# Kernel optimization log

Hardware: AMD Instinct MI355X
Metric: run time of the kernel (lower is better)

## Reference

```python
import jax, jax.numpy as jnp
import numpy as np

B, S, D = 16, 4096, 128
FACTOR = 1


def setup_inputs() -> dict:
    key = jax.random.key(0)
    kq, kk, kv = jax.random.split(key, 3)
    Q = jax.random.normal(kq, (B, S, D), dtype=jnp.float32)
    K = jax.random.normal(kk, (B, S, D), dtype=jnp.float32)
    V = jax.random.normal(kv, (B, S, D), dtype=jnp.float32)
    return {"Q": Q, "K": K, "V": V}


def reference(Q, K, V):
    # [B, S, D] -> [B, D, S] (head dim of 1 is elided; all ops are per-(b,d) lane)
    Qc = jnp.transpose(Q, (0, 2, 1))
    Kc = jnp.transpose(K, (0, 2, 1))
    Vc = jnp.transpose(V, (0, 2, 1))
    seq_len = Qc.shape[-1]
    # FFT cross-correlation: corr[b,d,tau] = sum_t Q[b,d,t] K[b,d,t-tau] (circular)
    corr = jnp.fft.irfft(
        jnp.fft.rfft(Qc, axis=-1) * jnp.conj(jnp.fft.rfft(Kc, axis=-1)),
        n=seq_len, axis=-1)  # [B, D, S]
    top_k = int(FACTOR * np.log(seq_len))  # = 8 for S=4096
    weights, delay = jax.lax.top_k(corr, top_k)  # [B, D, K], raw corr values (no softmax)
    # time-delay aggregation: roll V circularly by each selected delay and weighted-sum
    t = jnp.arange(seq_len)
    idx = (delay[..., None] + t[None, None, None, :]) % seq_len  # [B, D, K, S]
    pattern = jnp.take_along_axis(Vc[:, :, None, :], idx, axis=-1)  # [B, D, K, S]
    out = jnp.einsum('bdks,bdk->bds', pattern, weights)  # [B, D, S]
    # dropout is identity at inference
    return jnp.transpose(out, (0, 2, 1))  # [B, S, D]
```

## Files before the change

### kernel.cpp

```cpp
#include <hip/hip_runtime.h>
#include <math.h>

#define SEQ 4096
#define LOG2SEQ 12
#define TOPK 8
#define NB 16
#define ND 128
#define NEGINF (-3.402823466e+38f)

#define PADF(i) ((i) + ((i) >> 5))

__device__ __forceinline__ int rev12(int x) {
    return (int)(__brev((unsigned)x) >> (32 - LOG2SEQ));
}

__device__ __forceinline__ void transpose_body(const float* __restrict__ inb,
                                               float* __restrict__ outb,
                                               int R, int C) {
    __shared__ float tile[32][33];
    const int c0 = blockIdx.x * 32, r0 = blockIdx.y * 32;
#pragma unroll
    for (int j = 0; j < 32; j += 8) {
        tile[threadIdx.y + j][threadIdx.x] =
            inb[(size_t)(r0 + threadIdx.y + j) * C + (c0 + threadIdx.x)];
    }
    __syncthreads();
#pragma unroll
    for (int j = 0; j < 32; j += 8) {
        outb[(size_t)(c0 + threadIdx.y + j) * R + (r0 + threadIdx.x)] =
            tile[threadIdx.x][threadIdx.y + j];
    }
}

__global__ __launch_bounds__(256) void transpose3_k(const float* __restrict__ Q,
                                                    const float* __restrict__ K,
                                                    const float* __restrict__ V,
                                                    float* __restrict__ Qt,
                                                    float* __restrict__ Kt,
                                                    float* __restrict__ Vt) {
    const int which = blockIdx.z / NB;
    const int b = blockIdx.z % NB;
    const size_t bo = (size_t)b * SEQ * ND;
    const float* in = (which == 0) ? Q : (which == 1) ? K : V;
    float* out = (which == 0) ? Qt : (which == 1) ? Kt : Vt;
    transpose_body(in + bo, out + bo, SEQ, ND);
}

__global__ __launch_bounds__(256) void transpose_back_k(const float* __restrict__ in,
                                                        float* __restrict__ out) {
    const size_t bo = (size_t)blockIdx.z * SEQ * ND;
    transpose_body(in + bo, out + bo, ND, SEQ);
}

__global__ __launch_bounds__(256) void corr_topk_agg_k(const float* Qt,
                                                       const float* __restrict__ Kt,
                                                       const float* __restrict__ Vt,
                                                       float* Ot) {
    __shared__ float re[SEQ + SEQ / 32];
    __shared__ float im[SEQ + SEQ / 32];
    __shared__ float twc[SEQ / 2 + SEQ / 64];
    __shared__ float tws[SEQ / 2 + SEQ / 64];
    __shared__ float sval[4];
    __shared__ int sidx[4];
    __shared__ float wsel[TOPK];
    __shared__ int dsel[TOPK];

    const int tid = threadIdx.x;
    const size_t row = (size_t)blockIdx.x * SEQ;

    for (int j = tid; j < SEQ / 2; j += 256) {
        float s, c;
        sincosf(-6.283185307179586f * (float)j / (float)SEQ, &s, &c);
        twc[PADF(j)] = c;
        tws[PADF(j)] = s;
    }

    {
        const float4* Q4 = (const float4*)(Qt + row);
        const float4* K4 = (const float4*)(Kt + row);
        for (int t = tid; t < SEQ / 4; t += 256) {
            const float4 q = Q4[t];
            const float4 k = K4[t];
            const int b0 = PADF(4 * t);
            re[b0] = q.x; re[b0 + 1] = q.y; re[b0 + 2] = q.z; re[b0 + 3] = q.w;
            im[b0] = k.x; im[b0 + 1] = k.y; im[b0 + 2] = k.z; im[b0 + 3] = k.w;
        }
    }
    __syncthreads();

    for (int h = 2048; h >= 2; h >>= 2) {
        const int hh = h >> 1;
        const int sA = SEQ / (2 * h);
        for (int g = tid; g < SEQ / 4; g += 256) {
            const int pos = g & (hh - 1);
            const int i0 = ((g - pos) << 2) + pos;
            const int p0 = PADF(i0), p1 = PADF(i0 + hh);
            const int p2 = PADF(i0 + h), p3 = PADF(i0 + h + hh);
            const float e0r = re[p0], e0i = im[p0];
            const float e1r = re[p1], e1i = im[p1];
            const float e2r = re[p2], e2i = im[p2];
            const float e3r = re[p3], e3i = im[p3];
            const int ta = pos * sA;
            const int pta = PADF(ta), ptb = PADF(2 * ta);
            const float c1 = twc[pta], s1 = tws[pta];
            const float cB = twc[ptb], sB = tws[ptb];
            const float f0r = e0r + e2r, f0i = e0i + e2i;
            float dr = e0r - e2r, di = e0i - e2i;
            const float f2r = dr * c1 - di * s1, f2i = dr * s1 + di * c1;
            const float f1r = e1r + e3r, f1i = e1i + e3i;
            dr = e1r - e3r;
            di = e1i - e3i;
            const float f3r = dr * s1 + di * c1;
            const float f3i = di * s1 - dr * c1;
            re[p0] = f0r + f1r;
            im[p0] = f0i + f1i;
            dr = f0r - f1r;
            di = f0i - f1i;
            re[p1] = dr * cB - di * sB;
            im[p1] = dr * sB + di * cB;
            re[p2] = f2r + f3r;
            im[p2] = f2i + f3i;
            dr = f2r - f3r;
            di = f2i - f3i;
            re[p3] = dr * cB - di * sB;
            im[p3] = dr * sB + di * cB;
        }
        __syncthreads();
    }

    float ar_[9], ai_[9], br_[9], bi_[9];
#pragma unroll
    for (int q = 0; q < 9; ++q) {
        const int f = tid + (q << 8);
        if (f <= SEQ / 2) {
            const int pa = PADF(rev12(f));
            const int pb = PADF(rev12((SEQ - f) & (SEQ - 1)));
            ar_[q] = re[pa];
            ai_[q] = im[pa];
            br_[q] = re[pb];
            bi_[q] = im[pb];
        }
    }
    __syncthreads();
#pragma unroll
    for (int q = 0; q < 9; ++q) {
        const int f = tid + (q << 8);
        if (f <= SEQ / 2) {
            const float ar = ar_[q], ai = ai_[q], br = br_[q], bi = bi_[q];
            const float Qr = 0.5f * (ar + br), Qi = 0.5f * (ai - bi);
            const float Kr = 0.5f * (ai + bi), Ki = 0.5f * (br - ar);
            const float invS = 1.0f / (float)SEQ;
            const float Pr = (Qr * Kr + Qi * Ki) * invS;
            const float Pi = (Qi * Kr - Qr * Ki) * invS;
            const int pa = PADF(rev12(f));
            const int pb = PADF(rev12((SEQ - f) & (SEQ - 1)));
            re[pa] = Pr;
            im[pa] = Pi;
            re[pb] = Pr;
            im[pb] = -Pi;
        }
    }
    __syncthreads();

    for (int hh = 1; hh <= 1024; hh <<= 2) {
        const int sA = SEQ / (2 * hh);
        const int sB = SEQ / (4 * hh);
        for (int g = tid; g < SEQ / 4; g += 256) {
            const int pos = g & (hh - 1);
            const int i0 = ((g - pos) << 2) + pos;
            const int p0 = PADF(i0), p1 = PADF(i0 + hh);
            const int p2 = PADF(i0 + 2 * hh), p3 = PADF(i0 + 3 * hh);
            const float e0r = re[p0], e0i = im[p0];
            const float e1r = re[p1], e1i = im[p1];
            const float e2r = re[p2], e2i = im[p2];
            const float e3r = re[p3], e3i = im[p3];
            const int pta = PADF(pos * sA), ptb = PADF(pos * sB);
            const float cA = twc[pta], sAv = -tws[pta];
            const float cB = twc[ptb], sBv = -tws[ptb];
            float tr = e1r * cA - e1i * sAv, ti = e1r * sAv + e1i * cA;
            const float f0r = e0r + tr, f0i = e0i + ti;
            const float f1r = e0r - tr, f1i = e0i - ti;
            tr = e3r * cA - e3i * sAv;
            ti = e3r * sAv + e3i * cA;
            const float f2r = e2r + tr, f2i = e2i + ti;
            const float f3r = e2r - tr, f3i = e2i - ti;
            tr = f2r * cB - f2i * sBv;
            ti = f2r * sBv + f2i * cB;
            re[p0] = f0r + tr;
            im[p0] = f0i + ti;
            re[p2] = f0r - tr;
            im[p2] = f0i - ti;
            tr = -f3r * sBv - f3i * cB;
            ti = f3r * cB - f3i * sBv;
            re[p1] = f1r + tr;
            im[p1] = f1i + ti;
            re[p3] = f1r - tr;
            im[p3] = f1i - ti;
        }
        __syncthreads();
    }

    {
        const float4* V4 = (const float4*)(Vt + row);
        for (int t = tid; t < SEQ / 4; t += 256) {
            const float4 v = V4[t];
            const int b0 = PADF(4 * t);
            im[b0] = v.x; im[b0 + 1] = v.y; im[b0 + 2] = v.z; im[b0 + 3] = v.w;
        }
    }

    for (int it = 0; it < TOPK; ++it) {
        float best = NEGINF;
        int bidx = 0;
#pragma unroll
        for (int j = 0; j < SEQ / 256; ++j) {
            const int t = tid + (j << 8);
            const float v = re[PADF(t)];
            if (v > best) {
                best = v;
                bidx = t;
            }
        }
#pragma unroll
        for (int off = 32; off > 0; off >>= 1) {
            const float ov = __shfl_down(best, off);
            const int oi = __shfl_down(bidx, off);
            if (ov > best || (ov == best && oi < bidx)) {
                best = ov;
                bidx = oi;
            }
        }
        if ((tid & 63) == 0) {
            sval[tid >> 6] = best;
            sidx[tid >> 6] = bidx;
        }
        __syncthreads();
        if (tid == 0) {
            float bv = sval[0];
            int bi2 = sidx[0];
#pragma unroll
            for (int w = 1; w < 4; ++w) {
                const float ov = sval[w];
                const int oi = sidx[w];
                if (ov > bv || (ov == bv && oi < bi2)) {
                    bv = ov;
                    bi2 = oi;
                }
            }
            wsel[it] = bv;
            dsel[it] = bi2;
            re[PADF(bi2)] = NEGINF;
        }
        __syncthreads();
    }

    float w[TOPK];
    int dl[TOPK];
#pragma unroll
    for (int k = 0; k < TOPK; ++k) {
        w[k] = wsel[k];
        dl[k] = dsel[k];
    }
    for (int j = 0; j < SEQ / 256; ++j) {
        const int t = tid + (j << 8);
        float acc = 0.0f;
#pragma unroll
        for (int k = 0; k < TOPK; ++k) {
            acc += w[k] * im[PADF((t + dl[k]) & (SEQ - 1))];
        }
        Ot[row + t] = acc;
    }
}

extern "C" void kernel_launch(void* const* d_in, const int* in_sizes, int n_in,
                              void* d_out, int out_size, void* d_ws, size_t ws_size,
                              hipStream_t stream) {
    const float* Q = (const float*)d_in[0];
    const float* K = (const float*)d_in[1];
    const float* V = (const float*)d_in[2];
    float* out = (float*)d_out;

    const size_t n = (size_t)NB * ND * SEQ;
    float* Qt = (float*)d_ws;
    float* Kt = Qt + n;
    float* Vt = Kt + n;

    dim3 tb(32, 8, 1);

    dim3 g1(ND / 32, SEQ / 32, 3 * NB);
    hipLaunchKernelGGL(transpose3_k, g1, tb, 0, stream, Q, K, V, Qt, Kt, Vt);

    hipLaunchKernelGGL(corr_topk_agg_k, dim3(NB * ND), dim3(256), 0, stream,
                       Qt, Kt, Vt, Qt);

    dim3 g3(SEQ / 32, ND / 32, NB);
    hipLaunchKernelGGL(transpose_back_k, g3, tb, 0, stream, Qt, out);
}
```

Measured before the change: 259.0 us.

## Use 64x64 float4 transposes, compute FFT twiddles inline, keep top-k values in registers

The transpose kernels move to 64x64 tiles with float4 global loads and stores through a padded LDS tile, to get wider memory transactions. The FFT no longer fills shared twiddle tables: it computes one twiddle per butterfly with fast __sinf/__cosf and derives the second by angle doubling, which frees LDS and removes the table setup. Top-k selection caches the 16 candidate values per thread in registers and masks the winner there instead of rereading shared memory each round. The fast intrinsics and doubling formula lose some precision, which could change which lags top-k picks when correlation values are close.

```diff
diff --git a/kernel.cpp b/kernel.cpp
--- a/kernel.cpp
+++ b/kernel.cpp
@@ -10,25 +10,43 @@
 
 #define PADF(i) ((i) + ((i) >> 5))
 
+#define TPITCH 68
+
 __device__ __forceinline__ int rev12(int x) {
     return (int)(__brev((unsigned)x) >> (32 - LOG2SEQ));
 }
 
-__device__ __forceinline__ void transpose_body(const float* __restrict__ inb,
-                                               float* __restrict__ outb,
-                                               int R, int C) {
-    __shared__ float tile[32][33];
-    const int c0 = blockIdx.x * 32, r0 = blockIdx.y * 32;
-#pragma unroll
-    for (int j = 0; j < 32; j += 8) {
-        tile[threadIdx.y + j][threadIdx.x] =
-            inb[(size_t)(r0 + threadIdx.y + j) * C + (c0 + threadIdx.x)];
+__device__ __forceinline__ void twid(int idx, float& c, float& s) {
+    const float a = (float)idx * (-0.001533980787885641f);
+    c = __cosf(a);
+    s = __sinf(a);
+}
+
+__device__ __forceinline__ void transpose64_body(const float* __restrict__ inb,
+                                                 float* __restrict__ outb,
+                                                 int R, int C) {
+    __shared__ float lds[64 * TPITCH];
+    const int tid = threadIdx.x;
+    const int c0 = blockIdx.x * 64, r0 = blockIdx.y * 64;
+    const int q = tid & 15;
+    const int rr = tid >> 4;
+#pragma unroll
+    for (int pass = 0; pass < 4; ++pass) {
+        const int r = pass * 16 + rr;
+        const float4 v =
+            *(const float4*)(inb + (size_t)(r0 + r) * C + (c0 + 4 * q));
+        const int base = (4 * q) * TPITCH + r;
+        lds[base] = v.x;
+        lds[base + TPITCH] = v.y;
+        lds[base + 2 * TPITCH] = v.z;
+        lds[base + 3 * TPITCH] = v.w;
     }
     __syncthreads();
 #pragma unroll
-    for (int j = 0; j < 32; j += 8) {
-        outb[(size_t)(c0 + threadIdx.y + j) * R + (r0 + threadIdx.x)] =
-            tile[threadIdx.x][threadIdx.y + j];
+    for (int pass = 0; pass < 4; ++pass) {
+        const int c = pass * 16 + rr;
+        const float4 v = *(const float4*)(lds + c * TPITCH + 4 * q);
+        *(float4*)(outb + (size_t)(c0 + c) * R + (r0 + 4 * q)) = v;
     }
 }
 
@@ -43,13 +61,13 @@
     const size_t bo = (size_t)b * SEQ * ND;
     const float* in = (which == 0) ? Q : (which == 1) ? K : V;
     float* out = (which == 0) ? Qt : (which == 1) ? Kt : Vt;
-    transpose_body(in + bo, out + bo, SEQ, ND);
+    transpose64_body(in + bo, out + bo, SEQ, ND);
 }
 
 __global__ __launch_bounds__(256) void transpose_back_k(const float* __restrict__ in,
                                                         float* __restrict__ out) {
     const size_t bo = (size_t)blockIdx.z * SEQ * ND;
-    transpose_body(in + bo, out + bo, ND, SEQ);
+    transpose64_body(in + bo, out + bo, ND, SEQ);
 }
 
 __global__ __launch_bounds__(256) void corr_topk_agg_k(const float* Qt,
@@ -58,8 +76,6 @@
                                                        float* Ot) {
     __shared__ float re[SEQ + SEQ / 32];
     __shared__ float im[SEQ + SEQ / 32];
-    __shared__ float twc[SEQ / 2 + SEQ / 64];
-    __shared__ float tws[SEQ / 2 + SEQ / 64];
     __shared__ float sval[4];
     __shared__ int sidx[4];
     __shared__ float wsel[TOPK];
@@ -67,13 +83,6 @@
 
     const int tid = threadIdx.x;
     const size_t row = (size_t)blockIdx.x * SEQ;
-
-    for (int j = tid; j < SEQ / 2; j += 256) {
-        float s, c;
-        sincosf(-6.283185307179586f * (float)j / (float)SEQ, &s, &c);
-        twc[PADF(j)] = c;
-        tws[PADF(j)] = s;
-    }
 
     {
         const float4* Q4 = (const float4*)(Qt + row);
@@ -100,10 +109,10 @@
             const float e1r = re[p1], e1i = im[p1];
             const float e2r = re[p2], e2i = im[p2];
             const float e3r = re[p3], e3i = im[p3];
-            const int ta = pos * sA;
-            const int pta = PADF(ta), ptb = PADF(2 * ta);
-            const float c1 = twc[pta], s1 = tws[pta];
-            const float cB = twc[ptb], sB = tws[ptb];
+            float c1, s1;
+            twid(pos * sA, c1, s1);
+            const float cB = c1 * c1 - s1 * s1;
+            const float sB = 2.0f * s1 * c1;
             const float f0r = e0r + e2r, f0i = e0i + e2i;
             float dr = e0r - e2r, di = e0i - e2i;
             const float f2r = dr * c1 - di * s1, f2i = dr * s1 + di * c1;
@@ -163,7 +172,6 @@
     __syncthreads();
 
     for (int hh = 1; hh <= 1024; hh <<= 2) {
-        const int sA = SEQ / (2 * hh);
         const int sB = SEQ / (4 * hh);
         for (int g = tid; g < SEQ / 4; g += 256) {
             const int pos = g & (hh - 1);
@@ -174,9 +182,12 @@
             const float e1r = re[p1], e1i = im[p1];
             const float e2r = re[p2], e2i = im[p2];
             const float e3r = re[p3], e3i = im[p3];
-            const int pta = PADF(pos * sA), ptb = PADF(pos * sB);
-            const float cA = twc[pta], sAv = -tws[pta];
-            const float cB = twc[ptb], sBv = -tws[ptb];
+            float cB0, sB0;
+            twid(pos * sB, cB0, sB0);
+            const float cA = cB0 * cB0 - sB0 * sB0;
+            const float sAv = -2.0f * sB0 * cB0;
+            const float cB = cB0;
+            const float sBv = -sB0;
             float tr = e1r * cA - e1i * sAv, ti = e1r * sAv + e1i * cA;
             const float f0r = e0r + tr, f0i = e0i + ti;
             const float f1r = e0r - tr, f1i = e0i - ti;
@@ -209,15 +220,19 @@
         }
     }
 
+    float vals[16];
+#pragma unroll
+    for (int j = 0; j < 16; ++j) {
+        vals[j] = re[PADF(tid + (j << 8))];
+    }
     for (int it = 0; it < TOPK; ++it) {
         float best = NEGINF;
         int bidx = 0;
 #pragma unroll
-        for (int j = 0; j < SEQ / 256; ++j) {
+        for (int j = 0; j < 16; ++j) {
             const int t = tid + (j << 8);
-            const float v = re[PADF(t)];
-            if (v > best) {
-                best = v;
+            if (vals[j] > best) {
+                best = vals[j];
                 bidx = t;
             }
         }
@@ -249,9 +264,13 @@
             }
             wsel[it] = bv;
             dsel[it] = bi2;
-            re[PADF(bi2)] = NEGINF;
         }
         __syncthreads();
+        const int win = dsel[it];
+#pragma unroll
+        for (int j = 0; j < 16; ++j) {
+            if (tid + (j << 8) == win) vals[j] = NEGINF;
+        }
     }
 
     float w[TOPK];
@@ -285,14 +304,12 @@
     float* Kt = Qt + n;
     float* Vt = Kt + n;
 
-    dim3 tb(32, 8, 1);
-
-    dim3 g1(ND / 32, SEQ / 32, 3 * NB);
-    hipLaunchKernelGGL(transpose3_k, g1, tb, 0, stream, Q, K, V, Qt, Kt, Vt);
+    dim3 g1(ND / 64, SEQ / 64, 3 * NB);
+    hipLaunchKernelGGL(transpose3_k, g1, dim3(256), 0, stream, Q, K, V, Qt, Kt, Vt);
 
     hipLaunchKernelGGL(corr_topk_agg_k, dim3(NB * ND), dim3(256), 0, stream,
                        Qt, Kt, Vt, Qt);
 
-    dim3 g3(SEQ / 32, ND / 32, NB);
-    hipLaunchKernelGGL(transpose_back_k, g3, tb, 0, stream, Qt, out);
-}
+    dim3 g3(SEQ / 64, ND / 64, NB);
+    hipLaunchKernelGGL(transpose_back_k, g3, dim3(256), 0, stream, Qt, out);
+}
```

Result: faster. 242.3 us (-6.5%).
